# Kernel optimization log

Measured on AMD Instinct MI355X. Metric: run time of the kernel, lower is better.

The kernel has to match this reference:

```python
import jax, jax.numpy as jnp
import numpy as np

B, C, W, H = 16, 512, 64, 64
OUT, NH = 512, 8
HD = OUT // NH          # 64
K = 64                  # kernel_size == attended axis length (height)


def setup_inputs() -> dict:
    key = jax.random.key(0)
    k0, k1, k2, k3 = jax.random.split(key, 4)
    s = float(HD) ** -0.5
    return {
        "x": jax.random.normal(k0, (B, C, W, H), jnp.float32),
        "in_proj_weight": jax.random.normal(k1, (2 * OUT, C), jnp.float32) * s,
        "in_proj_bias": jnp.zeros((2 * OUT,), jnp.float32),
        "out_proj_w": jax.random.normal(k2, (OUT, OUT), jnp.float32) * s,
        "out_proj_b": jnp.zeros((OUT,), jnp.float32),
        "relative": jax.random.normal(k3, (2 * HD, 2 * K - 1), jnp.float32) * s,
    }


def reference(x, in_proj_weight, in_proj_bias, out_proj_w, out_proj_b, relative):
    b, c, w, h = x.shape
    hd2 = HD // 2
    # width=False, self-attention path: permute(0,3,2,1) then flat view
    xq = jnp.transpose(x, (0, 3, 2, 1)).reshape(b * w, h, c)
    qkv = xq @ in_proj_weight.T + in_proj_bias
    q, k, v = jnp.split(qkv, [OUT // 2, OUT], axis=2)

    # relative position embeddings gathered into [2*HD, K, K]
    rel_idx = jnp.arange(K)[:, None] - jnp.arange(K)[None, :] + (K - 1)  # key i, query j
    emb = relative[:, rel_idx]                                          # [2*HD, K, K]
    q_emb, k_emb, v_emb = jnp.split(emb, [hd2, HD], axis=0)

    # [bw, heads, ch, pos]
    q = q.reshape(b * w, h, NH, hd2).transpose(0, 2, 3, 1)
    k = k.reshape(b * w, h, NH, hd2).transpose(0, 2, 3, 1)
    v = v.reshape(b * w, h, NH, HD).transpose(0, 2, 3, 1)

    qr = jnp.einsum('bgci,cij->bgij', q, q_emb)
    kr = jnp.einsum('bgci,cij->bgij', k, k_emb).swapaxes(2, 3)
    qk = jnp.einsum('bgci,bgcj->bgij', q, k)
    sim = jax.nn.softmax(qk + qr + kr, axis=3)

    sv = jnp.einsum('bgij,bgcj->bgci', sim, v)     # [bw, NH, HD, h]
    sve = jnp.einsum('bgij,cij->bgci', sim, v_emb)  # [bw, NH, HD, h]
    out = (sv + sve).reshape(b * w, OUT, h).swapaxes(1, 2)  # [bw, h, OUT]
    out = out @ out_proj_w.T + out_proj_b
    # [b, w, h, OUT] -> transpose(2,3) -> permute(0,2,3,1) == transpose(0,3,2,1)
    out = out.reshape(b, w, h, OUT).transpose(0, 3, 2, 1)   # [B, OUT, H, W]
    return out
```

## Files before the change

### kernel.cpp

```cpp
#include <hip/hip_runtime.h>

using u16 = unsigned short;
using u32 = unsigned int;
typedef __attribute__((ext_vector_type(8))) _Float16 h8v;
typedef __attribute__((ext_vector_type(8))) u16 us8;
typedef __attribute__((ext_vector_type(2))) u32 u32x2;
typedef __attribute__((ext_vector_type(4))) float f4v;

__device__ __forceinline__ u16 f2h(float f) {
  _Float16 h = (_Float16)f;
  return __builtin_bit_cast(unsigned short, h);
}
__device__ __forceinline__ _Float16 bits2h(u16 u) {
  return __builtin_bit_cast(_Float16, u);
}

__device__ __forceinline__ f4v mfma16(h8v a, h8v b, f4v c) {
  return __builtin_amdgcn_mfma_f32_16x16x32_f16(a, b, c, 0, 0, 0);
}

__device__ __forceinline__ void gll16(const void* g, void* l) {
  __builtin_amdgcn_global_load_lds(
      (const __attribute__((address_space(1))) void*)g,
      (__attribute__((address_space(3))) void*)l, 16, 0, 0);
}


__global__ __launch_bounds__(256) void k0_setup(
    const float* __restrict__ w1, const float* __restrict__ wout,
    const float* __restrict__ rel, u16* __restrict__ W1b, u16* __restrict__ Woutb,
    u16* __restrict__ EqT, u16* __restrict__ EkT, u16* __restrict__ Evp)
{
  int idx = blockIdx.x * 256 + threadIdx.x;
  if (idx < 524288) {
    W1b[idx] = f2h(w1[idx]);
  } else if (idx < 786432) {
    int k = idx - 524288; Woutb[k] = f2h(wout[k]);
  } else if (idx < 790528) {
    int k = idx - 786432; int t = k >> 5, c = k & 31;
    EqT[k] = (t < 127) ? f2h(rel[c * 127 + t]) : (u16)0;
  } else if (idx < 794624) {
    int k = idx - 790528; int t = k >> 5, c = k & 31;
    EkT[k] = (t < 127) ? f2h(rel[(32 + c) * 127 + t]) : (u16)0;
  } else if (idx < 802816) {
    int k = idx - 794624; int c = k >> 7, t = k & 127;
    Evp[k] = (t < 127) ? f2h(rel[(64 + c) * 127 + t]) : (u16)0;
  }
}

__global__ __launch_bounds__(512, 2) void k1_qkv(
    const float* __restrict__ x, const u16* __restrict__ W1b,
    const float* __restrict__ bias, u16* __restrict__ qkv)
{
  __shared__ u16 POOL[65536];
  u16* XL = POOL;
  u16* WD = POOL + 32768;
  const int bid = blockIdx.x;
  const int b = bid >> 6, w = bid & 63;
  const int tid = threadIdx.x;
  const int l = tid & 63, wv = tid >> 6;
  const int lr = l & 15, lg = l >> 4;
  const int osub = wv * 64;

  auto stageB = [&](int ot, int kk, int buf) {
#pragma unroll
    for (int q = 0; q < 4; q++) {
      int slot = q * 512 + tid;
      int o = slot >> 2, c4 = slot & 3;
      gll16(W1b + (size_t)(ot * 512 + o) * 512 + kk * 32 +
                ((c4 ^ ((o >> 1) & 3)) << 3),
            WD + buf * 16384 + slot * 8);
    }
  };

  stageB(0, 0, 0);

  {
    const int r = tid & 63;
    const int cb = tid >> 6;
    const float* xb = x + ((size_t)b * 512 * 64 + w) * 64 + r;
#pragma unroll
    for (int q = 0; q < 8; q++) {
      int cc = (q << 3) | cb;
      float v[8];
#pragma unroll
      for (int e = 0; e < 8; e++)
        v[e] = xb[(size_t)(cc * 8 + e) * 4096];
      us8 o;
#pragma unroll
      for (int e = 0; e < 8; e++) o[e] = f2h(v[e]);
      *(us8*)&XL[r * 512 + ((cc ^ (r & 7)) << 3)] = o;
    }
  }
  __syncthreads();

  for (int ot = 0; ot < 2; ot++) {
    const int o0 = ot * 512;
    f4v acc[4][4];
#pragma unroll
    for (int mt = 0; mt < 4; mt++)
#pragma unroll
      for (int nt = 0; nt < 4; nt++) acc[mt][nt] = (f4v){0.f, 0.f, 0.f, 0.f};

#pragma unroll
    for (int kk = 0; kk < 16; kk++) {
      int cur = kk & 1;
      if (kk < 15) stageB(ot, kk + 1, cur ^ 1);
      h8v wf[4], xf[4];
#pragma unroll
      for (int mt = 0; mt < 4; mt++) {
        int o = osub + mt * 16 + lr;
        wf[mt] = *(const h8v*)&WD[cur * 16384 + o * 32 +
                                  ((lg ^ ((o >> 1) & 3)) << 3)];
      }
#pragma unroll
      for (int nt = 0; nt < 4; nt++) {
        int r = nt * 16 + lr;
        int cc = kk * 4 + lg;
        xf[nt] = *(const h8v*)&XL[r * 512 + ((cc ^ (r & 7)) << 3)];
      }
#pragma unroll
      for (int mt = 0; mt < 4; mt++)
#pragma unroll
        for (int nt = 0; nt < 4; nt++)
          acc[mt][nt] = mfma16(wf[mt], xf[nt], acc[mt][nt]);
      __syncthreads();
    }

    u16* Tr = WD;
    float4 bias4[4];
#pragma unroll
    for (int mt = 0; mt < 4; mt++)
      bias4[mt] = *(const float4*)&bias[o0 + osub + mt * 16 + lg * 4];
#pragma unroll
    for (int mt = 0; mt < 4; mt++)
#pragma unroll
      for (int nt = 0; nt < 4; nt++) {
        int r = nt * 16 + lr;
#pragma unroll
        for (int ep = 0; ep < 2; ep++) {
          int o_ = osub + mt * 16 + lg * 4 + 2 * ep;
          float v0 = acc[mt][nt][2 * ep + 0] + ((const float*)&bias4[mt])[2 * ep + 0];
          float v1 = acc[mt][nt][2 * ep + 1] + ((const float*)&bias4[mt])[2 * ep + 1];
          unsigned pk = (unsigned)f2h(v0) | ((unsigned)f2h(v1) << 16);
          int cc = o_ >> 3;
          int dst = (cc & 56) | ((cc & 7) ^ (r & 7));
          *(unsigned*)&Tr[r * 512 + dst * 8 + (o_ & 7)] = pk;
        }
      }
    __syncthreads();
#pragma unroll
    for (int p = 0; p < 8; p++) {
      int u = p * 512 + tid;
      int r = u >> 6, cc = u & 63;
      int dst = (cc & 56) | ((cc & 7) ^ (r & 7));
      us8 v = *(const us8*)&Tr[r * 512 + dst * 8];
      size_t S = (size_t)(b * 64 + r) * 64 + w;
      *(us8*)&qkv[S * 1024 + o0 + cc * 8] = v;
    }
    __syncthreads();
    if (ot == 0) { stageB(1, 0, 0); __syncthreads(); }
  }
}

__global__ __launch_bounds__(256) void k2_attn(
    const u16* __restrict__ qkv, const u16* __restrict__ EqT,
    const u16* __restrict__ EkT, const u16* __restrict__ Evp,
    u16* __restrict__ attn, int bid0)
{
  const int bid = blockIdx.x + bid0;
  const int s = bid >> 3, g = bid & 7;
  const int tid = threadIdx.x;
  const int l = tid & 63, wv = tid >> 6;
  const int lr = l & 15, lg = l >> 4;
  const int i0 = wv * 16;
  const u16* base = qkv + (size_t)s * 65536;

  __shared__ __align__(16) u16 POOL[16896];
  u16* QEi = POOL;
  u16* KEj = POOL + 8448;
  u16* Pl  = POOL;
  u16* VTl = POOL + 4096;
  u16* Psh = POOL + 8192;

  us8 vreg0, vreg1;
  {
    int u0 = tid,        j0_ = u0 >> 3, cb0 = u0 & 7;
    int u1 = tid + 256,  j1_ = u1 >> 3, cb1 = u1 & 7;
    vreg0 = *(const us8*)(base + j0_ * 1024 + 512 + g * 64 + cb0 * 8);
    vreg1 = *(const us8*)(base + j1_ * 1024 + 512 + g * 64 + cb1 * 8);
  }

  h8v qf = *(const h8v*)(base + (i0 + lr) * 1024 + g * 32 + lg * 8);
  h8v kf[4];
#pragma unroll
  for (int jt = 0; jt < 4; jt++)
    kf[jt] = *(const h8v*)(base + (jt * 16 + lr) * 1024 + 256 + g * 32 + lg * 8);

  const f4v z4 = {0.f, 0.f, 0.f, 0.f};

#pragma unroll
  for (int tt = 0; tt < 8; tt++) {
    h8v eb = *(const h8v*)(EqT + (tt * 16 + lr) * 32 + lg * 8);
    f4v d = mfma16(eb, qf, z4);
    int tb = tt * 16 + 4 * lg;
    u32x2 pk;
    pk[0] = (u32)f2h(d[0]) | ((u32)f2h(d[1]) << 16);
    pk[1] = (u32)f2h(d[2]) | ((u32)f2h(d[3]) << 16);
    *(u32x2*)&QEi[(i0 + lr) * 132 + tb] = pk;
  }
#pragma unroll
  for (int q = 0; q < 2; q++) {
    int tt = wv * 2 + q;
    h8v ea = *(const h8v*)(EkT + (tt * 16 + lr) * 32 + lg * 8);
#pragma unroll
    for (int jt = 0; jt < 4; jt++) {
      f4v d = mfma16(ea, kf[jt], z4);
      int tb = tt * 16 + 4 * lg;
      u32x2 pk;
      pk[0] = (u32)f2h(d[0]) | ((u32)f2h(d[1]) << 16);
      pk[1] = (u32)f2h(d[2]) | ((u32)f2h(d[3]) << 16);
      *(u32x2*)&KEj[(jt * 16 + lr) * 132 + tb] = pk;
    }
  }
  f4v sc[4];
#pragma unroll
  for (int jt = 0; jt < 4; jt++) sc[jt] = mfma16(kf[jt], qf, z4);

  __syncthreads();

  const int i = i0 + lr;
  float pv[4][4];
  {
    int qbase = i * 133 + 63 - 4 * lg;
    int kbase = 8448 + 4 * lg * 133 + 63 - i;
#pragma unroll
    for (int jt = 0; jt < 4; jt++)
#pragma unroll
      for (int e = 0; e < 4; e++) {
        float qr = (float)bits2h(POOL[qbase - 16 * jt - e]);
        float kr = (float)bits2h(POOL[kbase + 2128 * jt + 133 * e]);
        pv[jt][e] = sc[jt][e] + qr + kr;
      }
  }
  float inv;
  {
    float m = pv[0][0];
#pragma unroll
    for (int jt = 0; jt < 4; jt++)
#pragma unroll
      for (int e = 0; e < 4; e++) m = fmaxf(m, pv[jt][e]);
    m = fmaxf(m, __shfl_xor(m, 16));
    m = fmaxf(m, __shfl_xor(m, 32));
    float t0 = 0.f;
#pragma unroll
    for (int jt = 0; jt < 4; jt++)
#pragma unroll
      for (int e = 0; e < 4; e++) {
        pv[jt][e] = exp2f((pv[jt][e] - m) * 1.4426950408889634f);
        t0 += pv[jt][e];
      }
    t0 += __shfl_xor(t0, 16);
    t0 += __shfl_xor(t0, 32);
    inv = 1.f / t0;
  }
#pragma unroll
  for (int jt = 0; jt < 4; jt++)
#pragma unroll
    for (int e = 0; e < 4; e++) pv[jt][e] *= inv;

  __syncthreads();

#pragma unroll
  for (int jt = 0; jt < 4; jt++) {
    int j0 = jt * 16 + 4 * lg;
    int jc = j0 >> 3;
    u32x2 pk;
    pk[0] = (u32)f2h(pv[jt][0]) | ((u32)f2h(pv[jt][1]) << 16);
    pk[1] = (u32)f2h(pv[jt][2]) | ((u32)f2h(pv[jt][3]) << 16);
    *(u32x2*)&Pl[i * 64 + ((jc ^ (i & 7)) << 3) + (j0 & 7)] = pk;
#pragma unroll
    for (int e = 0; e < 4; e++) {
      int d = i + 63 - (j0 + e);
      int cd = d >> 3;
      Psh[i * 128 + (((cd & 8) | ((cd & 7) ^ (i & 7))) << 3) + (d & 7)] =
          f2h(pv[jt][e]);
    }
  }
  {
    int zi = tid >> 2;
#pragma unroll
    for (int kk = 0; kk < 16; kk++) {
      int k = (tid & 3) * 16 + kk;
      int col = (k < zi) ? k : (k + 64);
      int cd = col >> 3;
      Psh[zi * 128 + (((cd & 8) | ((cd & 7) ^ (zi & 7))) << 3) + (col & 7)] = 0;
    }
    int u0 = tid, j0_ = u0 >> 3, cb0 = u0 & 7;
#pragma unroll
    for (int e = 0; e < 8; e++) {
      int c = cb0 * 8 + e;
      VTl[c * 64 + (((j0_ >> 3) ^ (c & 7)) << 3) + (j0_ & 7)] = (u16)vreg0[e];
    }
    int u1 = tid + 256, j1_ = u1 >> 3, cb1 = u1 & 7;
#pragma unroll
    for (int e = 0; e < 8; e++) {
      int c = cb1 * 8 + e;
      VTl[c * 64 + (((j1_ >> 3) ^ (c & 7)) << 3) + (j1_ & 7)] = (u16)vreg1[e];
    }
  }
  __syncthreads();

  f4v acc[4] = {z4, z4, z4, z4};
  {
#pragma unroll
    for (int kc = 0; kc < 2; kc++) {
      h8v pa = *(const h8v*)&Pl[i * 64 + (((kc * 4 + lg) ^ (i & 7)) << 3)];
#pragma unroll
      for (int ct = 0; ct < 4; ct++) {
        int cA = ct * 16 + lr;
        h8v vb = *(const h8v*)&VTl[cA * 64 + (((kc * 4 + lg) ^ (cA & 7)) << 3)];
        acc[ct] = mfma16(pa, vb, acc[ct]);
      }
    }
#pragma unroll
    for (int tc = 0; tc < 4; tc++) {
      int cd = tc * 4 + lg;
      int cds = (cd & 8) | ((cd & 7) ^ (i & 7));
      h8v pa = *(const h8v*)&Psh[i * 128 + cds * 8];
#pragma unroll
      for (int ct = 0; ct < 4; ct++) {
        h8v eb = *(const h8v*)(Evp + (ct * 16 + lr) * 128 + tc * 32 + lg * 8);
        acc[ct] = mfma16(pa, eb, acc[ct]);
      }
    }
  }
#pragma unroll
  for (int ct = 0; ct < 4; ct++)
#pragma unroll
    for (int r = 0; r < 4; r++) {
      int io = i0 + lg * 4 + r;
      attn[(size_t)(s * 64 + io) * 512 + g * 64 + ct * 16 + lr] = f2h(acc[ct][r]);
    }
}

__global__ __launch_bounds__(512) void k3_oproj(
    const u16* __restrict__ attn, const u16* __restrict__ Woutb,
    const float* __restrict__ ob, float* __restrict__ out)
{
  const int bid = blockIdx.x;
  const int b = bid >> 6, w = bid & 63;
  const int tid = threadIdx.x;
  const int l = tid & 63, wv = tid >> 6;
  const int lr = l & 15, lg = l >> 4;

  __shared__ u16 Bl[2][64 * 64];

  f4v acc[4][4];
#pragma unroll
  for (int a_ = 0; a_ < 4; a_++)
#pragma unroll
    for (int b_ = 0; b_ < 4; b_++) acc[a_][b_] = (f4v){0.f, 0.f, 0.f, 0.f};

  auto stageB = [&](int kk, int buf) {
    int c0 = kk * 64;
    int h_l = wv * 8 + (l >> 3);
    int p = l & 7;
    const u16* src = attn + ((size_t)b * 4096 + (size_t)h_l * 64 + w) * 512 + c0 +
                     ((p ^ (h_l & 7)) << 3);
    gll16(src, &Bl[buf][wv * 512]);
  };

  stageB(0, 0);
  __syncthreads();

  for (int kk = 0; kk < 8; kk++) {
    int cur = kk & 1, nxt = cur ^ 1;
    if (kk < 7) stageB(kk + 1, nxt);
    int c0 = kk * 64;
    h8v af[4][2], bf[4][2];
#pragma unroll
    for (int mt = 0; mt < 4; mt++)
#pragma unroll
      for (int kc = 0; kc < 2; kc++)
        af[mt][kc] = *(const h8v*)(Woutb + (size_t)(wv * 64 + mt * 16 + lr) * 512 +
                                   c0 + kc * 32 + lg * 8);
#pragma unroll
    for (int jt = 0; jt < 4; jt++)
#pragma unroll
      for (int kc = 0; kc < 2; kc++) {
        int h = jt * 16 + lr;
        bf[jt][kc] = *(const h8v*)&Bl[cur][h * 64 + (((kc * 4 + lg) ^ (h & 7)) << 3)];
      }
#pragma unroll
    for (int mt = 0; mt < 4; mt++)
#pragma unroll
      for (int jt = 0; jt < 4; jt++)
#pragma unroll
        for (int kc = 0; kc < 2; kc++)
          acc[mt][jt] = mfma16(af[mt][kc], bf[jt][kc], acc[mt][jt]);
    __syncthreads();
  }

#pragma unroll
  for (int mt = 0; mt < 4; mt++)
#pragma unroll
    for (int jt = 0; jt < 4; jt++)
#pragma unroll
      for (int e = 0; e < 4; e++) {
        int o = wv * 64 + mt * 16 + lg * 4 + e;
        int h = jt * 16 + lr;
        out[(((size_t)b * 512 + o) * 64 + w) * 64 + h] = acc[mt][jt][e] + ob[o];
      }
}

extern "C" void kernel_launch(void* const* d_in, const int* in_sizes, int n_in,
                              void* d_out, int out_size, void* d_ws, size_t ws_size,
                              hipStream_t stream)
{
  (void)in_sizes; (void)n_in; (void)out_size; (void)ws_size;
  const float* x    = (const float*)d_in[0];
  const float* w1   = (const float*)d_in[1];
  const float* b1   = (const float*)d_in[2];
  const float* wout = (const float*)d_in[3];
  const float* bo   = (const float*)d_in[4];
  const float* rel  = (const float*)d_in[5];
  float* out = (float*)d_out;

  char* ws = (char*)d_ws;
  u16* qkv_ws  = (u16*)ws;
  u16* attn_ws = (u16*)(ws + 134217728);
  u16* W1b     = (u16*)(ws + 201326592);
  u16* Woutb   = (u16*)(ws + 202375168);
  u16* EqT     = (u16*)(ws + 202899456);
  u16* EkT     = (u16*)(ws + 202907648);
  u16* Evp     = (u16*)(ws + 202915840);

  k0_setup<<<dim3(3136), dim3(256), 0, stream>>>(w1, wout, rel, W1b, Woutb, EqT, EkT, Evp);
  k1_qkv  <<<dim3(1024), dim3(512), 0, stream>>>(x, W1b, b1, qkv_ws);
  k2_attn <<<dim3(4096), dim3(256), 0, stream>>>(qkv_ws, EqT, EkT, Evp, attn_ws, 0);
  k2_attn <<<dim3(4096), dim3(256), 0, stream>>>(qkv_ws, EqT, EkT, Evp, attn_ws, 4096);
  k3_oproj<<<dim3(1024), dim3(512), 0, stream>>>(attn_ws, Woutb, bo, out);
}
```

Measured before the change: 358.6 us.

## Load QKV weights directly from global into registers, drop LDS weight staging

The QKV projection kernel no longer double-buffers weight tiles through shared memory with a barrier per k-step. Each wave now owns 128 output rows across the full 1024-wide output and reads its weight fragments straight from global memory, relying on cache reuse across blocks. Both output halves come from one accumulation pass, and shared-memory use is halved, which could allow more resident blocks. In exchange, the larger accumulator and fragment arrays raise register pressure and spill risk, and weight loads become less coalesced, per-lane global reads.

```diff
diff --git a/kernel.cpp b/kernel.cpp
--- a/kernel.cpp
+++ b/kernel.cpp
@@ -52,28 +52,14 @@
     const float* __restrict__ x, const u16* __restrict__ W1b,
     const float* __restrict__ bias, u16* __restrict__ qkv)
 {
-  __shared__ u16 POOL[65536];
+  __shared__ u16 POOL[32768];
   u16* XL = POOL;
-  u16* WD = POOL + 32768;
   const int bid = blockIdx.x;
   const int b = bid >> 6, w = bid & 63;
   const int tid = threadIdx.x;
   const int l = tid & 63, wv = tid >> 6;
   const int lr = l & 15, lg = l >> 4;
-  const int osub = wv * 64;
-
-  auto stageB = [&](int ot, int kk, int buf) {
-#pragma unroll
-    for (int q = 0; q < 4; q++) {
-      int slot = q * 512 + tid;
-      int o = slot >> 2, c4 = slot & 3;
-      gll16(W1b + (size_t)(ot * 512 + o) * 512 + kk * 32 +
-                ((c4 ^ ((o >> 1) & 3)) << 3),
-            WD + buf * 16384 + slot * 8);
-    }
-  };
-
-  stageB(0, 0, 0);
+  const int O0 = wv * 128;
 
   {
     const int r = tid & 63;
@@ -94,60 +80,68 @@
   }
   __syncthreads();
 
-  for (int ot = 0; ot < 2; ot++) {
-    const int o0 = ot * 512;
-    f4v acc[4][4];
-#pragma unroll
-    for (int mt = 0; mt < 4; mt++)
-#pragma unroll
-      for (int nt = 0; nt < 4; nt++) acc[mt][nt] = (f4v){0.f, 0.f, 0.f, 0.f};
-
-#pragma unroll
-    for (int kk = 0; kk < 16; kk++) {
-      int cur = kk & 1;
-      if (kk < 15) stageB(ot, kk + 1, cur ^ 1);
-      h8v wf[4], xf[4];
-#pragma unroll
-      for (int mt = 0; mt < 4; mt++) {
-        int o = osub + mt * 16 + lr;
-        wf[mt] = *(const h8v*)&WD[cur * 16384 + o * 32 +
-                                  ((lg ^ ((o >> 1) & 3)) << 3)];
-      }
-#pragma unroll
-      for (int nt = 0; nt < 4; nt++) {
+  f4v acc[8][4];
+#pragma unroll
+  for (int mt = 0; mt < 8; mt++)
+#pragma unroll
+    for (int nt = 0; nt < 4; nt++) acc[mt][nt] = (f4v){0.f, 0.f, 0.f, 0.f};
+
+  const u16* Wb = W1b + (size_t)(O0 + lr) * 512 + lg * 8;
+#pragma unroll 1
+  for (int kk = 0; kk < 8; kk++) {
+    h8v af[8][2];
+#pragma unroll
+    for (int mt = 0; mt < 8; mt++)
+#pragma unroll
+      for (int kc = 0; kc < 2; kc++)
+        af[mt][kc] = *(const h8v*)(Wb + (size_t)(mt * 16) * 512 + kk * 64 + kc * 32);
+    h8v xf[4][2];
+#pragma unroll
+    for (int nt = 0; nt < 4; nt++)
+#pragma unroll
+      for (int kc = 0; kc < 2; kc++) {
         int r = nt * 16 + lr;
-        int cc = kk * 4 + lg;
-        xf[nt] = *(const h8v*)&XL[r * 512 + ((cc ^ (r & 7)) << 3)];
-      }
-#pragma unroll
-      for (int mt = 0; mt < 4; mt++)
-#pragma unroll
-        for (int nt = 0; nt < 4; nt++)
-          acc[mt][nt] = mfma16(wf[mt], xf[nt], acc[mt][nt]);
-      __syncthreads();
-    }
-
-    u16* Tr = WD;
-    float4 bias4[4];
-#pragma unroll
-    for (int mt = 0; mt < 4; mt++)
-      bias4[mt] = *(const float4*)&bias[o0 + osub + mt * 16 + lg * 4];
-#pragma unroll
-    for (int mt = 0; mt < 4; mt++)
-#pragma unroll
-      for (int nt = 0; nt < 4; nt++) {
-        int r = nt * 16 + lr;
-#pragma unroll
-        for (int ep = 0; ep < 2; ep++) {
-          int o_ = osub + mt * 16 + lg * 4 + 2 * ep;
-          float v0 = acc[mt][nt][2 * ep + 0] + ((const float*)&bias4[mt])[2 * ep + 0];
-          float v1 = acc[mt][nt][2 * ep + 1] + ((const float*)&bias4[mt])[2 * ep + 1];
-          unsigned pk = (unsigned)f2h(v0) | ((unsigned)f2h(v1) << 16);
-          int cc = o_ >> 3;
-          int dst = (cc & 56) | ((cc & 7) ^ (r & 7));
-          *(unsigned*)&Tr[r * 512 + dst * 8 + (o_ & 7)] = pk;
+        int cc = kk * 8 + kc * 4 + lg;
+        xf[nt][kc] = *(const h8v*)&XL[r * 512 + ((cc ^ (r & 7)) << 3)];
+      }
+#pragma unroll
+    for (int mt = 0; mt < 8; mt++)
+#pragma unroll
+      for (int nt = 0; nt < 4; nt++)
+#pragma unroll
+        for (int kc = 0; kc < 2; kc++)
+          acc[mt][nt] = mfma16(af[mt][kc], xf[nt][kc], acc[mt][nt]);
+  }
+  __syncthreads();
+
+  u16* Tr = POOL;
+  float4 bias4[8];
+#pragma unroll
+  for (int mt = 0; mt < 8; mt++)
+    bias4[mt] = *(const float4*)&bias[O0 + mt * 16 + lg * 4];
+
+  const int hhw = wv >> 2;
+  const int ow = (wv & 3) * 128;
+#pragma unroll
+  for (int hh = 0; hh < 2; hh++) {
+    if (hhw == hh) {
+#pragma unroll
+      for (int mt = 0; mt < 8; mt++)
+#pragma unroll
+        for (int nt = 0; nt < 4; nt++) {
+          int r = nt * 16 + lr;
+#pragma unroll
+          for (int ep = 0; ep < 2; ep++) {
+            int o_ = ow + mt * 16 + lg * 4 + 2 * ep;
+            float v0 = acc[mt][nt][2 * ep + 0] + ((const float*)&bias4[mt])[2 * ep + 0];
+            float v1 = acc[mt][nt][2 * ep + 1] + ((const float*)&bias4[mt])[2 * ep + 1];
+            unsigned pk = (unsigned)f2h(v0) | ((unsigned)f2h(v1) << 16);
+            int cc = o_ >> 3;
+            int dst = (cc & 56) | ((cc & 7) ^ (r & 7));
+            *(unsigned*)&Tr[r * 512 + dst * 8 + (o_ & 7)] = pk;
+          }
         }
-      }
+    }
     __syncthreads();
 #pragma unroll
     for (int p = 0; p < 8; p++) {
@@ -156,10 +150,9 @@
       int dst = (cc & 56) | ((cc & 7) ^ (r & 7));
       us8 v = *(const us8*)&Tr[r * 512 + dst * 8];
       size_t S = (size_t)(b * 64 + r) * 64 + w;
-      *(us8*)&qkv[S * 1024 + o0 + cc * 8] = v;
-    }
-    __syncthreads();
-    if (ot == 0) { stageB(1, 0, 0); __syncthreads(); }
+      *(us8*)&qkv[S * 1024 + hh * 512 + cc * 8] = v;
+    }
+    if (hh == 0) __syncthreads();
   }
 }
 
```

Result: slower. 382.2 us (+6.6%).
